# Optimization experiments

Measured on AMD Instinct MI355X. Metric: run time of the kernel, lower is better.

Reference implementation:

```python
import jax, jax.numpy as jnp
import numpy as np

P1, P2 = 100003, 1009  # spatial hash primes from the torch source
D = 16  # block_dim (stage-3 BLOCK_DIM)

FACE_OFFSETS = jnp.array([[-1,0,0],[1,0,0],[0,-1,0],[0,1,0],[0,0,-1],[0,0,1]], dtype=jnp.int32)
NEIGHBOR_OFFSETS = jnp.array([
    [-1,0,0],[1,0,0],[0,-1,0],[0,1,0],[0,0,-1],[0,0,1],
    [-1,-1,0],[-1,1,0],[1,-1,0],[1,1,0],
    [-1,0,-1],[-1,0,1],[1,0,-1],[1,0,1],
    [0,-1,-1],[0,-1,1],[0,1,-1],[0,1,1],
    [-1,-1,-1],[-1,-1,1],[-1,1,-1],[-1,1,1],
    [1,-1,-1],[1,-1,1],[1,1,-1],[1,1,1]], dtype=jnp.int32)


def _face_dists_flat(d):
    # [d^3, 6] distance of each in-block voxel to the 6 block faces, in [0,1]
    lin = jnp.linspace(0.0, 1.0, d)
    gx, gy, gz = jnp.meshgrid(lin, lin, lin, indexing='ij')
    return jnp.stack([gx, 1.0 - gx, gy, 1.0 - gy, gz, 1.0 - gz], axis=-1).reshape(-1, 6)


def _match(xyz, offsets):
    # xyz: [N,3] int32 block coords of one batch; offsets: [K,3]
    # returns [N,K] bool: does a block exist at xyz+offset (hash sort + searchsorted)
    n = xyz.shape[0]
    keys = xyz[:, 0] * P1 + xyz[:, 1] * P2 + xyz[:, 2]
    sorted_keys = jnp.sort(keys)
    nb = xyz[:, None, :] + offsets[None, :, :]               # [N,K,3]
    nbk = (nb[..., 0] * P1 + nb[..., 1] * P2 + nb[..., 2]).reshape(-1)
    pos = jnp.clip(jnp.searchsorted(sorted_keys, nbk), 0, n - 1)
    return (sorted_keys[pos] == nbk).reshape(n, offsets.shape[0])


def setup_inputs() -> dict:
    key = jax.random.key(0)
    # [B, N, 3] block coords (batch dim explicit, equal per-batch layout)
    coords = jax.random.randint(key, (4, 2048, 3), 0, 64, dtype=jnp.int32)
    return {"coords": coords}


def reference(coords):
    face_flat = _face_dists_flat(D)                           # [D^3, 6]
    has_nb = jax.vmap(lambda x: _match(x, FACE_OFFSETS))(coords)       # [B,N,6]
    # face without a neighbor keeps its boundary distance; else distance 1.0
    prior = jnp.min(jnp.where(has_nb[:, :, None, :], 1.0, face_flat[None, None, :, :]), axis=-1)  # [B,N,D^3]
    occ = jax.vmap(lambda x: _match(x, NEIGHBOR_OFFSETS))(coords).astype(jnp.float32)             # [B,N,26]
    return prior, occ
```

## Files before the change

### kernel.cpp

```cpp
#include <hip/hip_runtime.h>


#define B 4
#define N 2048
#define BM_WORDS 8192
#define PRIOR_ELEMS (4ull * 2048ull * 4096ull)

static __device__ __constant__ int NB_OFF[26][3] = {
    {-1,0,0},{1,0,0},{0,-1,0},{0,1,0},{0,0,-1},{0,0,1},
    {-1,-1,0},{-1,1,0},{1,-1,0},{1,1,0},
    {-1,0,-1},{-1,0,1},{1,0,-1},{1,0,1},
    {0,-1,-1},{0,-1,1},{0,1,-1},{0,1,1},
    {-1,-1,-1},{-1,-1,1},{-1,1,-1},{-1,1,1},
    {1,-1,-1},{1,-1,1},{1,1,-1},{1,1,1}
};

__device__ __forceinline__ bool bm_test(const unsigned* bm, int x, int y, int z) {
    if (((x | y | z) & ~63) != 0) return false;
    unsigned idx = ((unsigned)x << 12) | ((unsigned)y << 6) | (unsigned)z;
    return (bm[idx >> 5] >> (idx & 31u)) & 1u;
}

__global__ void scatter_bits(const int* __restrict__ coords, unsigned* __restrict__ bm) {
    int id = blockIdx.x * blockDim.x + threadIdx.x;
    if (id >= B * N) return;
    int b = id >> 11;
    int x = coords[id * 3 + 0];
    int y = coords[id * 3 + 1];
    int z = coords[id * 3 + 2];
    unsigned idx = ((unsigned)x << 12) | ((unsigned)y << 6) | (unsigned)z;
    atomicOr(&bm[b * BM_WORDS + (idx >> 5)], 1u << (idx & 31u));
}

__global__ void __launch_bounds__(256)
compute_outputs(const int* __restrict__ coords, const unsigned* __restrict__ bm,
                float* __restrict__ out) {
    int pid = blockIdx.x;
    int tid = threadIdx.x;
    int b = pid >> 11;
    const unsigned* bmb = bm + b * BM_WORDS;

    int x = coords[pid * 3 + 0];
    int y = coords[pid * 3 + 1];
    int z = coords[pid * 3 + 2];

    bool nxm = bm_test(bmb, x - 1, y, z);
    bool nxp = bm_test(bmb, x + 1, y, z);
    bool nym = bm_test(bmb, x, y - 1, z);
    bool nyp = bm_test(bmb, x, y + 1, z);
    bool nzm = bm_test(bmb, x, y, z - 1);
    bool nzp = bm_test(bmb, x, y, z + 1);

    const float inv15 = 1.0f / 15.0f;
    float4* outp = (float4*)(out + (size_t)pid * 4096);

    #pragma unroll
    for (int j = 0; j < 4; ++j) {
        int v4 = j * 256 + tid;
        int v = v4 * 4;
        int ix = (v >> 8) & 15;
        int iy = (v >> 4) & 15;
        int iz0 = v & 15;
        float gx = ix * inv15;
        float gy = iy * inv15;
        float m = 1.0f;
        if (!nxm) m = fminf(m, gx);
        if (!nxp) m = fminf(m, 1.0f - gx);
        if (!nym) m = fminf(m, gy);
        if (!nyp) m = fminf(m, 1.0f - gy);
        float r[4];
        #pragma unroll
        for (int k = 0; k < 4; ++k) {
            float gz = (iz0 + k) * inv15;
            float mm = m;
            if (!nzm) mm = fminf(mm, gz);
            if (!nzp) mm = fminf(mm, 1.0f - gz);
            r[k] = mm;
        }
        outp[v4] = make_float4(r[0], r[1], r[2], r[3]);
    }

    if (tid < 26) {
        bool hit = bm_test(bmb, x + NB_OFF[tid][0], y + NB_OFF[tid][1], z + NB_OFF[tid][2]);
        out[PRIOR_ELEMS + (size_t)pid * 26 + tid] = hit ? 1.0f : 0.0f;
    }
}

extern "C" void kernel_launch(void* const* d_in, const int* in_sizes, int n_in,
                              void* d_out, int out_size, void* d_ws, size_t ws_size,
                              hipStream_t stream) {
    const int* coords = (const int*)d_in[0];
    float* out = (float*)d_out;
    unsigned* bm = (unsigned*)d_ws;

    hipMemsetAsync(bm, 0, (size_t)B * BM_WORDS * sizeof(unsigned), stream);

    scatter_bits<<<(B * N + 255) / 256, 256, 0, stream>>>(coords, bm);
    compute_outputs<<<B * N, 256, 0, stream>>>(coords, bm, out);
}
```

Measured before the change: 137.7 us.

## Fuse bitmap build and output kernels, building per-block shared-memory bitmap

Replaces the memset, scatter kernel and per-point output kernel with one fused kernel. Each block rebuilds its batch's occupancy bitmap in shared memory and then processes 8 points. This removes the global bitmap, the extra launches and the global bitmap reads. In exchange, every block redundantly zeroes 32KB of shared memory and scatters all 2048 coordinates with atomics, and the shared memory use limits occupancy.

Result: no change. 137.2 us (-0.3%).

```diff
diff --git a/kernel.cpp b/kernel.cpp
--- a/kernel.cpp
+++ b/kernel.cpp
@@ -3,6 +3,8 @@
 
 #define B 4
 #define N 2048
+#define PPB 8
+#define BLOCKS_PER_BATCH (N / PPB)
 #define BM_WORDS 8192
 #define PRIOR_ELEMS (4ull * 2048ull * 4096ull)
 
@@ -21,68 +23,76 @@
     return (bm[idx >> 5] >> (idx & 31u)) & 1u;
 }
 
-__global__ void scatter_bits(const int* __restrict__ coords, unsigned* __restrict__ bm) {
-    int id = blockIdx.x * blockDim.x + threadIdx.x;
-    if (id >= B * N) return;
-    int b = id >> 11;
-    int x = coords[id * 3 + 0];
-    int y = coords[id * 3 + 1];
-    int z = coords[id * 3 + 2];
-    unsigned idx = ((unsigned)x << 12) | ((unsigned)y << 6) | (unsigned)z;
-    atomicOr(&bm[b * BM_WORDS + (idx >> 5)], 1u << (idx & 31u));
-}
+__global__ void __launch_bounds__(256, 4)
+fused_kernel(const int* __restrict__ coords, float* __restrict__ out) {
+    __shared__ unsigned bm[BM_WORDS];
+    __shared__ unsigned char fex[PPB][6];
 
-__global__ void __launch_bounds__(256)
-compute_outputs(const int* __restrict__ coords, const unsigned* __restrict__ bm,
-                float* __restrict__ out) {
-    int pid = blockIdx.x;
-    int tid = threadIdx.x;
-    int b = pid >> 11;
-    const unsigned* bmb = bm + b * BM_WORDS;
+    const int tid = threadIdx.x;
+    const int blk = blockIdx.x;
+    const int b = blk / BLOCKS_PER_BATCH;
+    const int p0 = (blk % BLOCKS_PER_BATCH) * PPB;
+    const int* cb = coords + b * N * 3;
 
-    int x = coords[pid * 3 + 0];
-    int y = coords[pid * 3 + 1];
-    int z = coords[pid * 3 + 2];
+    for (int i = tid; i < BM_WORDS; i += 256) bm[i] = 0u;
+    __syncthreads();
 
-    bool nxm = bm_test(bmb, x - 1, y, z);
-    bool nxp = bm_test(bmb, x + 1, y, z);
-    bool nym = bm_test(bmb, x, y - 1, z);
-    bool nyp = bm_test(bmb, x, y + 1, z);
-    bool nzm = bm_test(bmb, x, y, z - 1);
-    bool nzp = bm_test(bmb, x, y, z + 1);
+    for (int i = tid; i < N; i += 256) {
+        int x = cb[3 * i + 0];
+        int y = cb[3 * i + 1];
+        int z = cb[3 * i + 2];
+        unsigned idx = ((unsigned)x << 12) | ((unsigned)y << 6) | (unsigned)z;
+        atomicOr(&bm[idx >> 5], 1u << (idx & 31u));
+    }
+    __syncthreads();
+
+    if (tid < PPB * 6) {
+        int p = tid / 6, f = tid % 6;
+        int x = cb[3 * (p0 + p) + 0];
+        int y = cb[3 * (p0 + p) + 1];
+        int z = cb[3 * (p0 + p) + 2];
+        fex[p][f] = bm_test(bm, x + NB_OFF[f][0], y + NB_OFF[f][1], z + NB_OFF[f][2]) ? 1 : 0;
+    }
+    if (tid < PPB * 26) {
+        int p = tid / 26, k = tid % 26;
+        int x = cb[3 * (p0 + p) + 0];
+        int y = cb[3 * (p0 + p) + 1];
+        int z = cb[3 * (p0 + p) + 2];
+        float hit = bm_test(bm, x + NB_OFF[k][0], y + NB_OFF[k][1], z + NB_OFF[k][2]) ? 1.0f : 0.0f;
+        out[PRIOR_ELEMS + (size_t)(b * N + p0) * 26 + tid] = hit;
+    }
+    __syncthreads();
 
     const float inv15 = 1.0f / 15.0f;
-    float4* outp = (float4*)(out + (size_t)pid * 4096);
-
     #pragma unroll
-    for (int j = 0; j < 4; ++j) {
-        int v4 = j * 256 + tid;
-        int v = v4 * 4;
-        int ix = (v >> 8) & 15;
-        int iy = (v >> 4) & 15;
-        int iz0 = v & 15;
-        float gx = ix * inv15;
-        float gy = iy * inv15;
-        float m = 1.0f;
-        if (!nxm) m = fminf(m, gx);
-        if (!nxp) m = fminf(m, 1.0f - gx);
-        if (!nym) m = fminf(m, gy);
-        if (!nyp) m = fminf(m, 1.0f - gy);
-        float r[4];
+    for (int p = 0; p < PPB; ++p) {
+        bool nxm = fex[p][0], nxp = fex[p][1];
+        bool nym = fex[p][2], nyp = fex[p][3];
+        bool nzm = fex[p][4], nzp = fex[p][5];
+        float4* outp = (float4*)(out + (size_t)(b * N + p0 + p) * 4096);
         #pragma unroll
-        for (int k = 0; k < 4; ++k) {
-            float gz = (iz0 + k) * inv15;
-            float mm = m;
-            if (!nzm) mm = fminf(mm, gz);
-            if (!nzp) mm = fminf(mm, 1.0f - gz);
-            r[k] = mm;
+        for (int j = 0; j < 4; ++j) {
+            int v4 = j * 256 + tid;
+            int v = v4 * 4;
+            float gx = (float)((v >> 8) & 15) * inv15;
+            float gy = (float)((v >> 4) & 15) * inv15;
+            int iz0 = v & 15;
+            float m = 1.0f;
+            if (!nxm) m = fminf(m, gx);
+            if (!nxp) m = fminf(m, 1.0f - gx);
+            if (!nym) m = fminf(m, gy);
+            if (!nyp) m = fminf(m, 1.0f - gy);
+            float r[4];
+            #pragma unroll
+            for (int k = 0; k < 4; ++k) {
+                float gz = (float)(iz0 + k) * inv15;
+                float mm = m;
+                if (!nzm) mm = fminf(mm, gz);
+                if (!nzp) mm = fminf(mm, 1.0f - gz);
+                r[k] = mm;
+            }
+            outp[v4] = make_float4(r[0], r[1], r[2], r[3]);
         }
-        outp[v4] = make_float4(r[0], r[1], r[2], r[3]);
-    }
-
-    if (tid < 26) {
-        bool hit = bm_test(bmb, x + NB_OFF[tid][0], y + NB_OFF[tid][1], z + NB_OFF[tid][2]);
-        out[PRIOR_ELEMS + (size_t)pid * 26 + tid] = hit ? 1.0f : 0.0f;
     }
 }
 
@@ -91,10 +101,5 @@
                               hipStream_t stream) {
     const int* coords = (const int*)d_in[0];
     float* out = (float*)d_out;
-    unsigned* bm = (unsigned*)d_ws;
-
-    hipMemsetAsync(bm, 0, (size_t)B * BM_WORDS * sizeof(unsigned), stream);
-
-    scatter_bits<<<(B * N + 255) / 256, 256, 0, stream>>>(coords, bm);
-    compute_outputs<<<B * N, 256, 0, stream>>>(coords, bm, out);
+    fused_kernel<<<B * N / PPB, 256, 0, stream>>>(coords, out);
 }
```
